# Optimization experiments

Measured on AMD Instinct MI355X. Metric: run time of the kernel, lower is better.

## Reference

```python
import jax, jax.numpy as jnp
import numpy as np

# Fixed production-scale sizes (equal-sized graphs so unbatch == reshape)
B, NQ, ND = 64, 32, 512     # graph pairs, query nodes/graph, data nodes/graph
DIN, D, K = 64, 128, 16     # GCN_in_size, GCN_out_size, NTN_k
DEG = 8                     # average degree


def _gcn(x, src, dst, W, b):
    """GCNConv with self loops + symmetric normalization (PyG semantics)."""
    N = x.shape[0]
    loop = jnp.arange(N)
    s = jnp.concatenate([src, loop])
    t = jnp.concatenate([dst, loop])
    deg = jax.ops.segment_sum(jnp.ones_like(t, x.dtype), t, num_segments=N)
    dinv = jnp.where(deg > 0, deg ** -0.5, 0.0)
    norm = (dinv[s] * dinv[t])[:, None]
    h = x @ W
    return jax.ops.segment_sum(h[s] * norm, t, num_segments=N) + b


def _three_gcn(x, ei, W1, b1, W2, b2, W3, b3):
    src, dst = ei[0], ei[1]
    h1 = jax.nn.relu(_gcn(x, src, dst, W1, b1))
    h2 = jax.nn.relu(_gcn(h1, src, dst, W2, b2))
    h3 = jax.nn.relu(_gcn(h2, src, dst, W3, b3))
    return h1, h2, h3


def _level(q, d, Wn, Vn, bn, cw, cb):
    """att_layer + NTN + elementwise mult + 1x1 conv + softmax over data nodes.
    q: [B,NQ,D], d: [B,ND,D] -> (softmaxed map [B,NQ,ND], raw map, he [B,K,NQ,ND])."""
    att = jax.nn.softmax(jnp.einsum('bqd,bnd->bqn', q, d) / jnp.sqrt(jnp.float32(D)), axis=-1)
    qW = jnp.einsum('bqd,kde->bkqe', q, Wn)           # [B,K,NQ,D]
    bil = jnp.einsum('bkqe,bne->bkqn', qW, d)          # [B,K,NQ,ND]
    lq = jnp.einsum('kd,bqd->bkq', Vn[:, :D], q)[:, :, :, None]
    ld = jnp.einsum('kd,bnd->bkn', Vn[:, D:], d)[:, :, None, :]
    he = jax.nn.sigmoid(bil + lq + ld + bn[None, :, None, None]) * att[:, None]
    e_raw = jnp.einsum('k,bkqn->bqn', cw, he) + cb     # 1x1 Conv2d(K->1)
    return jax.nn.softmax(e_raw, axis=-1), e_raw, he


def reference(x_d, edge_index_d, x_q, edge_index_q, batch_index_d, batch_index_q,
              W1, b1, W2, b2, W3, b3,
              Wn1, Vn1, bn1, cw1, cb1,
              Wn2, Vn2, bn2, cw2, cb2,
              Wn3, Vn3, bn3, cw3, cb3,
              w_end, b_end):
    d1, d2, d3 = _three_gcn(x_d, edge_index_d, W1, b1, W2, b2, W3, b3)
    q1, q2, q3 = _three_gcn(x_q, edge_index_q, W1, b1, W2, b2, W3, b3)
    # unbatch: batch indices are sorted with equal graph sizes -> reshape
    d1, d2, d3 = (t.reshape(B, ND, D) for t in (d1, d2, d3))
    q1, q2, q3 = (t.reshape(B, NQ, D) for t in (q1, q2, q3))
    e1, _, he1 = _level(q1, d1, Wn1, Vn1, bn1, cw1, cb1)
    _, e2raw, he2 = _level(q2, d2, Wn2, Vn2, bn2, cw2, cb2)
    e3, _, he3 = _level(q3, d3, Wn3, Vn3, bn3, cw3, cb3)
    # Faithful to source quirks: the zip unpack `e1,e2,e3,h1,h2,h1` rebinds h1 to
    # he_3 (he_1 is never used, he_3 appears twice) and end2 enters the concat
    # PRE-softmax (the softmaxed version was assigned to unused `nd2`).
    stack = jnp.concatenate([e1[:, None], e2raw[:, None], e3[:, None], he3, he2, he3], axis=1)
    out = jnp.einsum('c,bcqn->bqn', w_end, stack) + b_end  # con_end 1x1 conv + squeeze
    return jax.nn.softmax(out, axis=-1)                    # softmax over data nodes


def setup_inputs() -> dict:
    key = jax.random.key(0)
    k = jax.random.split(key, 40)
    n = jax.random.normal
    Nd, Nq = B * ND, B * NQ
    Ed, Eq = Nd * DEG, Nq * DEG
    gid_d = jnp.repeat(jnp.arange(B), ND * DEG)
    gid_q = jnp.repeat(jnp.arange(B), NQ * DEG)
    inp = {
        'x_d': n(k[0], (Nd, DIN), jnp.float32),
        'x_q': n(k[1], (Nq, DIN), jnp.float32),
        'edge_index_d': jnp.stack([jax.random.randint(k[2], (Ed,), 0, ND) + gid_d * ND,
                                   jax.random.randint(k[3], (Ed,), 0, ND) + gid_d * ND]),
        'edge_index_q': jnp.stack([jax.random.randint(k[4], (Eq,), 0, NQ) + gid_q * NQ,
                                   jax.random.randint(k[5], (Eq,), 0, NQ) + gid_q * NQ]),
        'batch_index_d': jnp.repeat(jnp.arange(B), ND),
        'batch_index_q': jnp.repeat(jnp.arange(B), NQ),
        'W1': n(k[6], (DIN, D), jnp.float32) / np.sqrt(DIN), 'b1': jnp.zeros((D,), jnp.float32),
        'W2': n(k[7], (D, D), jnp.float32) / np.sqrt(D), 'b2': jnp.zeros((D,), jnp.float32),
        'W3': n(k[8], (D, D), jnp.float32) / np.sqrt(D), 'b3': jnp.zeros((D,), jnp.float32),
    }
    for i, l in enumerate(('1', '2', '3')):
        inp['Wn' + l] = n(k[10 + 4 * i], (K, D, D), jnp.float32) / np.sqrt(D)
        inp['Vn' + l] = n(k[11 + 4 * i], (K, 2 * D), jnp.float32) / np.sqrt(2 * D)
        inp['bn' + l] = jnp.zeros((K,), jnp.float32)
        inp['cw' + l] = n(k[12 + 4 * i], (K,), jnp.float32) / np.sqrt(K)
        inp['cb' + l] = jnp.zeros((1,), jnp.float32)
    inp['w_end'] = n(k[25], (3 * K + 3,), jnp.float32) / np.sqrt(3 * K + 3)
    inp['b_end'] = jnp.zeros((1,), jnp.float32)
    return inp
```

## Files before the change

kernel.cpp:

```cpp
#include <hip/hip_runtime.h>
#include <math.h>

namespace {
constexpr int cB  = 64;
constexpr int cNQ = 32;
constexpr int cND = 512;
constexpr int cNd = cB * cND;
constexpr int cNq = cB * cNQ;
constexpr int cEd = cNd * 8;
constexpr int cEq = cNq * 8;
constexpr int LD_STRIDE = 516;
constexpr int NB_CSRD = 64;
constexpr int NB_CSRQ = 8;
constexpr int CVT0 = NB_CSRD + NB_CSRQ;
constexpr int NB_CVT = 2188;
constexpr int TR0 = CVT0 + NB_CVT;
constexpr int NB_T2BF = 808;
constexpr int GA_N = 4352;
constexpr int QW_N = 1024;
}

#define F4C(p) (*(const float4*)(p))

typedef __attribute__((ext_vector_type(8))) __bf16 bf16x8;
typedef __attribute__((ext_vector_type(4))) float floatx4;

__device__ __forceinline__ ushort f2bf(float f) {
  union { float f; unsigned u; } v;
  v.f = f;
  unsigned u = v.u;
  return (ushort)((u + 0x7fffu + ((u >> 16) & 1u)) >> 16);
}
__device__ __forceinline__ float bf2f(ushort u) {
  union { unsigned u; float f; } v;
  v.u = ((unsigned)u) << 16;
  return v.f;
}
__device__ __forceinline__ float4 us4f4(ushort4 u) {
  return make_float4(bf2f(u.x), bf2f(u.y), bf2f(u.z), bf2f(u.w));
}
__device__ __forceinline__ ushort4 f4us4(float4 f) {
  ushort4 o;
  o.x = f2bf(f.x); o.y = f2bf(f.y); o.z = f2bf(f.z); o.w = f2bf(f.w);
  return o;
}
__device__ __forceinline__ float fexp2(float x) {
#if __has_builtin(__builtin_amdgcn_exp2f)
  return __builtin_amdgcn_exp2f(x);
#else
  return exp2f(x);
#endif
}
__device__ __forceinline__ float frcp(float x) {
#if __has_builtin(__builtin_amdgcn_rcpf)
  return __builtin_amdgcn_rcpf(x);
#else
  return 1.0f / x;
#endif
}
__device__ __forceinline__ float fsigmoid(float z) {
  return frcp(1.0f + fexp2(z * -1.4426950408889634f));
}
__device__ __forceinline__ float fexp(float x) { return fexp2(x * 1.4426950408889634f); }

__device__ __forceinline__ int swz_g(int j) { return (((j >> 3) & 7) << 3) | (j & 7); }

__global__ __launch_bounds__(256) void k_front_csr(
    const float* __restrict__ xd, const float* __restrict__ xq,
    const float* __restrict__ v0, const float* __restrict__ v1,
    const float* __restrict__ v2, ushort* __restrict__ oxd, ushort* __restrict__ oxq,
    ushort* __restrict__ ov0, ushort* __restrict__ ov1, ushort* __restrict__ ov2,
    const float* __restrict__ W1, const float* __restrict__ W2,
    const float* __restrict__ W3, const float* __restrict__ Wn0,
    const float* __restrict__ Wn1, const float* __restrict__ Wn2,
    ushort* __restrict__ o1, ushort* __restrict__ o2, ushort* __restrict__ o3,
    ushort* __restrict__ on0, ushort* __restrict__ on1, ushort* __restrict__ on2,
    const int* __restrict__ src_d, const int* __restrict__ dst_d,
    const int* __restrict__ src_q, const int* __restrict__ dst_q,
    int* __restrict__ cnt_d, int* __restrict__ cnt_q,
    int* __restrict__ rp_d, int* __restrict__ rp_q,
    float* __restrict__ dinv_d, float* __restrict__ dinv_q,
    int* __restrict__ col_d, int* __restrict__ col_q) {
  __shared__ float tile[32][33];
  __shared__ int s_cnt[512];
  __shared__ int s_base[512];
  __shared__ int s_cur[512];
  int blk = blockIdx.x, tid = threadIdx.x;
  if (blk < NB_CSRD) {
    int g = blk;
    const int* dstg = dst_d + g * 4096;
    const int* srcg = src_d + g * 4096;
    int nbase = g * 512;
    s_cnt[tid] = 0; s_cnt[tid + 256] = 0;
    __syncthreads();
    for (int e = tid; e < 4096; e += 256) atomicAdd(&s_cnt[dstg[e] - nbase], 1);
    __syncthreads();
    int c0 = s_cnt[tid], c1 = s_cnt[tid + 256];
    s_base[tid] = c0; s_base[tid + 256] = c1;
    __syncthreads();
    for (int off = 1; off < 512; off <<= 1) {
      int a = (tid >= off) ? s_base[tid - off] : 0;
      int b = (tid + 256 >= off) ? s_base[tid + 256 - off] : 0;
      __syncthreads();
      s_base[tid] += a; s_base[tid + 256] += b;
      __syncthreads();
    }
    int e0 = s_base[tid] - c0, e1 = s_base[tid + 256] - c1;
    s_base[tid] = e0; s_base[tid + 256] = e1;
    s_cur[tid] = 0; s_cur[tid + 256] = 0;
    cnt_d[nbase + tid] = c0;
    cnt_d[nbase + tid + 256] = c1;
    rp_d[nbase + tid] = g * 4096 + e0;
    rp_d[nbase + tid + 256] = g * 4096 + e1;
    dinv_d[nbase + tid] = 1.0f / sqrtf((float)(c0 + 1));
    dinv_d[nbase + tid + 256] = 1.0f / sqrtf((float)(c1 + 1));
    __syncthreads();
    for (int e = tid; e < 4096; e += 256) {
      int d = dstg[e] - nbase;
      int p = atomicAdd(&s_cur[d], 1);
      col_d[g * 4096 + s_base[d] + p] = srcg[e];
    }
  } else if (blk < CVT0) {
    int qb = blk - NB_CSRD;
    int lg = tid >> 5, lane32 = tid & 31;
    int g = qb * 8 + lg;
    const int* dstg = dst_q + g * 256;
    const int* srcg = src_q + g * 256;
    int nbase = g * 32;
    s_cnt[tid] = 0;
    __syncthreads();
#pragma unroll
    for (int j = 0; j < 8; ++j)
      atomicAdd(&s_cnt[lg * 32 + (dstg[lane32 + j * 32] - nbase)], 1);
    __syncthreads();
    int v = s_cnt[tid];
    int incl = v;
#pragma unroll
    for (int off = 1; off < 32; off <<= 1) {
      int t = __shfl_up(incl, off, 32);
      if (lane32 >= off) incl += t;
    }
    int excl = incl - v;
    cnt_q[nbase + lane32] = v;
    rp_q[nbase + lane32] = g * 256 + excl;
    dinv_q[nbase + lane32] = 1.0f / sqrtf((float)(v + 1));
    s_base[tid] = excl;
    s_cur[tid] = 0;
    __syncthreads();
#pragma unroll
    for (int j = 0; j < 8; ++j) {
      int e = lane32 + j * 32;
      int d = dstg[e] - nbase;
      int p = atomicAdd(&s_cur[lg * 32 + d], 1);
      col_q[g * 256 + s_base[lg * 32 + d] + p] = srcg[e];
    }
  } else if (blk < TR0) {
    int b2 = blk - CVT0;
    const float* src;
    ushort* dst;
    int i;
    if (b2 < 2048) { src = xd; dst = oxd; i = b2 * 256 + tid; }
    else if (b2 < 2176) { src = xq; dst = oxq; i = (b2 - 2048) * 256 + tid; }
    else if (b2 < 2180) { src = v0; dst = ov0; i = (b2 - 2176) * 256 + tid; }
    else if (b2 < 2184) { src = v1; dst = ov1; i = (b2 - 2180) * 256 + tid; }
    else { src = v2; dst = ov2; i = (b2 - 2184) * 256 + tid; }
    *(ushort4*)(dst + (size_t)i * 4) = f4us4(F4C(src + (size_t)i * 4));
  } else {
    int b5 = blk - TR0;
    const float* in;
    ushort* out;
    int R, C, bt, t;
    if (b5 < 8)        { in = W1;  out = o1;  R = 64;  C = 128; bt = 0; t = b5; }
    else if (b5 < 24)  { in = W2;  out = o2;  R = 128; C = 128; bt = 0; t = b5 - 8; }
    else if (b5 < 40)  { in = W3;  out = o3;  R = 128; C = 128; bt = 0; t = b5 - 24; }
    else if (b5 < 296) { in = Wn0; out = on0; R = 128; C = 128; bt = (b5 - 40) >> 4;  t = (b5 - 40) & 15; }
    else if (b5 < 552) { in = Wn1; out = on1; R = 128; C = 128; bt = (b5 - 296) >> 4; t = (b5 - 296) & 15; }
    else               { in = Wn2; out = on2; R = 128; C = 128; bt = (b5 - 552) >> 4; t = (b5 - 552) & 15; }
    int tilesC = C >> 5;
    int tr = t / tilesC, tc = t - tr * tilesC;
    int tx = tid & 31, ty = tid >> 5;
    const float* ib = in + (size_t)bt * R * C;
    ushort* ob = out + (size_t)bt * R * C;
#pragma unroll
    for (int i = 0; i < 4; ++i)
      tile[ty + i * 8][tx] = ib[(tr * 32 + ty + i * 8) * C + tc * 32 + tx];
    __syncthreads();
#pragma unroll
    for (int i = 0; i < 4; ++i)
      ob[(size_t)(tc * 32 + ty + i * 8) * R + tr * 32 + tx] = f2bf(tile[tx][ty + i * 8]);
  }
}

__global__ __launch_bounds__(256) void k_gemm1(
    const ushort* __restrict__ xdbf, const ushort* __restrict__ xqbf,
    const ushort* __restrict__ w1T, const float* __restrict__ dinv_d,
    const float* __restrict__ dinv_q, ushort* __restrict__ htmp) {
  int blk2 = blockIdx.x, tid = threadIdx.x;
  int wave = tid >> 6, lane = tid & 63;
  int col = lane & 15, quad = lane >> 4;
  bool isQ = blk2 >= 512;
  int node0;
  if (isQ) node0 = (blk2 - 512) * 64;
  else node0 = swz_g(blk2) * 512 + (blk2 >> 6) * 64;
  int mloc = node0 + wave * 16;
  const ushort* X = isQ ? xqbf : xdbf;
  const float* dv = isQ ? dinv_q : dinv_d;
  size_t hbase = isQ ? (size_t)cNd : 0;
  floatx4 acc[8];
#pragma unroll
  for (int ct = 0; ct < 8; ++ct)
#pragma unroll
    for (int r = 0; r < 4; ++r) acc[ct][r] = 0.0f;
#pragma unroll
  for (int kc = 0; kc < 2; ++kc) {
    bf16x8 a = *(const bf16x8*)(X + (size_t)(mloc + col) * 64 + kc * 32 + quad * 8);
#pragma unroll
    for (int ct = 0; ct < 8; ++ct) {
      bf16x8 b = *(const bf16x8*)(w1T + (size_t)(ct * 16 + col) * 64 + kc * 32 + quad * 8);
      acc[ct] = __builtin_amdgcn_mfma_f32_16x16x32_bf16(a, b, acc[ct], 0, 0, 0);
    }
  }
  float sc[4];
#pragma unroll
  for (int r = 0; r < 4; ++r) sc[r] = dv[mloc + quad * 4 + r];
#pragma unroll
  for (int ct = 0; ct < 8; ++ct)
#pragma unroll
    for (int r = 0; r < 4; ++r)
      htmp[(hbase + mloc + quad * 4 + r) * 128 + ct * 16 + col] = f2bf(acc[ct][r] * sc[r]);
}

__global__ __launch_bounds__(256) void k_gather_qw(
    const ushort* __restrict__ htmp, const int* __restrict__ rp_d,
    const int* __restrict__ cnt_d, const int* __restrict__ col_d,
    const float* __restrict__ dinv_d, const int* __restrict__ rp_q,
    const int* __restrict__ cnt_q, const int* __restrict__ col_q,
    const float* __restrict__ dinv_q, const float* __restrict__ bias,
    ushort* __restrict__ dbf, ushort* __restrict__ qbf,
    const ushort* __restrict__ wnT, ushort* __restrict__ qw) {
  __shared__ ushort q_s[32 * 128];
  int blk = blockIdx.x, tid = threadIdx.x;
  if (blk < GA_N) {
    bool isQ = blk >= 4096;
    int node;
    if (isQ) {
      int j = blk - 4096;
      node = swz_g(j) * 32 + (j >> 6) * 8 + (tid >> 5);
    } else {
      node = swz_g(blk) * 512 + (blk >> 6) * 8 + (tid >> 5);
    }
    int l = tid & 31;
    const ushort* hs = htmp + (isQ ? (size_t)cNd * 128 : 0);
    const int* rp = isQ ? rp_q : rp_d;
    const int* cnt = isQ ? cnt_q : cnt_d;
    const int* col = isQ ? col_q : col_d;
    const float* dinv = isQ ? dinv_q : dinv_d;
    ushort* outp = isQ ? qbf : dbf;
    int c = cnt[node], s0 = rp[node];
    float dt = dinv[node];
    float4 acc = us4f4(*(const ushort4*)(hs + (size_t)node * 128 + l * 4));
    int cm = c < 32 ? c : 32;
    for (int j0 = 0; j0 < cm; j0 += 8) {
      int ss[8];
      ushort4 v[8];
#pragma unroll
      for (int t = 0; t < 8; ++t) {
        int jj = j0 + t;
        ss[t] = (jj < cm) ? col[s0 + jj] : -1;
      }
#pragma unroll
      for (int t = 0; t < 8; ++t)
        if (ss[t] >= 0) v[t] = *(const ushort4*)(hs + (size_t)ss[t] * 128 + l * 4);
#pragma unroll
      for (int t = 0; t < 8; ++t) {
        if (ss[t] >= 0) {
          float4 f = us4f4(v[t]);
          acc.x += f.x; acc.y += f.y; acc.z += f.z; acc.w += f.w;
        }
      }
    }
    for (int j = 32; j < c; ++j) {
      int s = col[s0 + j];
      float4 f = us4f4(*(const ushort4*)(hs + (size_t)s * 128 + l * 4));
      acc.x += f.x; acc.y += f.y; acc.z += f.z; acc.w += f.w;
    }
    float4 bv = F4C(bias + l * 4);
    float4 r;
    r.x = fmaxf(acc.x * dt + bv.x, 0.0f);
    r.y = fmaxf(acc.y * dt + bv.y, 0.0f);
    r.z = fmaxf(acc.z * dt + bv.z, 0.0f);
    r.w = fmaxf(acc.w * dt + bv.w, 0.0f);
    *(ushort4*)(outp + (size_t)node * 128 + l * 4) = f4us4(r);
    return;
  }
  int j = blk - GA_N;
  int b = swz_g(j & 63), k = j >> 6;
  {
    int n = tid >> 3, seg = tid & 7, d0 = seg * 16;
    int node = b * 32 + n;
    int c = cnt_q[node], s0 = rp_q[node];
    float dt = dinv_q[node];
    const ushort* hq = htmp + (size_t)cNd * 128;
    const ushort* own = hq + (size_t)node * 128 + d0;
    float4 a0 = us4f4(*(const ushort4*)(own));
    float4 a1 = us4f4(*(const ushort4*)(own + 4));
    float4 a2 = us4f4(*(const ushort4*)(own + 8));
    float4 a3 = us4f4(*(const ushort4*)(own + 12));
    for (int j2 = 0; j2 < c; ++j2) {
      int s = col_q[s0 + j2];
      const ushort* rr = hq + (size_t)s * 128 + d0;
      float4 f0 = us4f4(*(const ushort4*)(rr));
      float4 f1 = us4f4(*(const ushort4*)(rr + 4));
      float4 f2 = us4f4(*(const ushort4*)(rr + 8));
      float4 f3 = us4f4(*(const ushort4*)(rr + 12));
      a0.x += f0.x; a0.y += f0.y; a0.z += f0.z; a0.w += f0.w;
      a1.x += f1.x; a1.y += f1.y; a1.z += f1.z; a1.w += f1.w;
      a2.x += f2.x; a2.y += f2.y; a2.z += f2.z; a2.w += f2.w;
      a3.x += f3.x; a3.y += f3.y; a3.z += f3.z; a3.w += f3.w;
    }
    float4 bv0 = F4C(bias + d0), bv1 = F4C(bias + d0 + 4);
    float4 bv2 = F4C(bias + d0 + 8), bv3 = F4C(bias + d0 + 12);
    float4 r0, r1, r2, r3;
    r0.x = fmaxf(a0.x * dt + bv0.x, 0.0f); r0.y = fmaxf(a0.y * dt + bv0.y, 0.0f);
    r0.z = fmaxf(a0.z * dt + bv0.z, 0.0f); r0.w = fmaxf(a0.w * dt + bv0.w, 0.0f);
    r1.x = fmaxf(a1.x * dt + bv1.x, 0.0f); r1.y = fmaxf(a1.y * dt + bv1.y, 0.0f);
    r1.z = fmaxf(a1.z * dt + bv1.z, 0.0f); r1.w = fmaxf(a1.w * dt + bv1.w, 0.0f);
    r2.x = fmaxf(a2.x * dt + bv2.x, 0.0f); r2.y = fmaxf(a2.y * dt + bv2.y, 0.0f);
    r2.z = fmaxf(a2.z * dt + bv2.z, 0.0f); r2.w = fmaxf(a2.w * dt + bv2.w, 0.0f);
    r3.x = fmaxf(a3.x * dt + bv3.x, 0.0f); r3.y = fmaxf(a3.y * dt + bv3.y, 0.0f);
    r3.z = fmaxf(a3.z * dt + bv3.z, 0.0f); r3.w = fmaxf(a3.w * dt + bv3.w, 0.0f);
    ushort4 u0 = f4us4(r0), u1 = f4us4(r1), u2 = f4us4(r2), u3 = f4us4(r3);
    char* qsb = (char*)q_s;
    int x0 = (n * 256 + d0 * 2) ^ ((n & 7) << 4);
    int x1 = (n * 256 + d0 * 2 + 16) ^ ((n & 7) << 4);
    *(ushort4*)(qsb + x0) = u0;
    *(ushort4*)(qsb + x0 + 8) = u1;
    *(ushort4*)(qsb + x1) = u2;
    *(ushort4*)(qsb + x1 + 8) = u3;
  }
  __syncthreads();
  int wave = tid >> 6, lane = tid & 63;
  int col = lane & 15, quad = lane >> 4;
  int et0 = wave * 2;
  const char* qsb = (const char*)q_s;
  floatx4 acc[2][2];
#pragma unroll
  for (int qt = 0; qt < 2; ++qt)
#pragma unroll
    for (int ei = 0; ei < 2; ++ei)
#pragma unroll
      for (int r = 0; r < 4; ++r) acc[qt][ei][r] = 0.0f;
#pragma unroll
  for (int kc = 0; kc < 4; ++kc) {
    int r0 = col, r1 = 16 + col;
    bf16x8 a0 = *(const bf16x8*)(qsb + ((r0 * 256 + kc * 64 + quad * 16) ^ ((r0 & 7) << 4)));
    bf16x8 a1 = *(const bf16x8*)(qsb + ((r1 * 256 + kc * 64 + quad * 16) ^ ((r1 & 7) << 4)));
#pragma unroll
    for (int ei = 0; ei < 2; ++ei) {
      bf16x8 bf = *(const bf16x8*)(wnT + (size_t)(k * 128 + (et0 + ei) * 16 + col) * 128 +
                                   kc * 32 + quad * 8);
      acc[0][ei] = __builtin_amdgcn_mfma_f32_16x16x32_bf16(a0, bf, acc[0][ei], 0, 0, 0);
      acc[1][ei] = __builtin_amdgcn_mfma_f32_16x16x32_bf16(a1, bf, acc[1][ei], 0, 0, 0);
    }
  }
#pragma unroll
  for (int qt = 0; qt < 2; ++qt)
#pragma unroll
    for (int ei = 0; ei < 2; ++ei)
#pragma unroll
      for (int r = 0; r < 4; ++r)
        qw[((size_t)(b * 16 + k) << 12) + (qt * 16 + quad * 4 + r) * 128 +
           (et0 + ei) * 16 + col] = f2bf(acc[qt][ei][r]);
}

__global__ __launch_bounds__(512, 2) void k_level_gemm(
    const ushort* __restrict__ qbf, const ushort* __restrict__ dbf,
    const ushort* __restrict__ qw, const ushort* __restrict__ vnbf,
    const float* __restrict__ bn, const float* __restrict__ cw,
    const float* __restrict__ w_end, const float* __restrict__ b_end,
    int o1, int o2, int hasF, int do_sm, int mode, int widx,
    float* __restrict__ accb, float* __restrict__ out,
    const ushort* __restrict__ gWT, const float* __restrict__ dinv_d,
    const float* __restrict__ dinv_q, ushort* __restrict__ htmp) {
  __shared__ float s_ld[16 * LD_STRIDE];
  __shared__ float s_lq[16 * 16];
  __shared__ float s_red[16 * 8];
  int tid = threadIdx.x;
  int wave = tid >> 6, lane = tid & 63;
  int col = lane & 15, quad = lane >> 4;

  if (blockIdx.x >= 128) {
    int gblk = blockIdx.x - 128;
    bool isQ = gblk >= 256;
    int node0;
    if (isQ) node0 = (gblk - 256) * 128;
    else node0 = swz_g(gblk) * 512 + (gblk >> 6) * 128;
    int mloc = node0 + wave * 16;
    const ushort* X = isQ ? qbf : dbf;
    const float* dv = isQ ? dinv_q : dinv_d;
    size_t hbase = isQ ? (size_t)cNd : 0;
    floatx4 acc[8];
#pragma unroll
    for (int ct = 0; ct < 8; ++ct)
#pragma unroll
      for (int r = 0; r < 4; ++r) acc[ct][r] = 0.0f;
#pragma unroll
    for (int kc = 0; kc < 4; ++kc) {
      bf16x8 a = *(const bf16x8*)(X + (size_t)(mloc + col) * 128 + kc * 32 + quad * 8);
#pragma unroll
      for (int ct = 0; ct < 8; ++ct) {
        bf16x8 b = *(const bf16x8*)(gWT + (size_t)(ct * 16 + col) * 128 + kc * 32 + quad * 8);
        acc[ct] = __builtin_amdgcn_mfma_f32_16x16x32_bf16(a, b, acc[ct], 0, 0, 0);
      }
    }
    float sc[4];
#pragma unroll
    for (int r = 0; r < 4; ++r) sc[r] = dv[mloc + quad * 4 + r];
#pragma unroll
    for (int ct = 0; ct < 8; ++ct)
#pragma unroll
      for (int r = 0; r < 4; ++r)
        htmp[(hbase + mloc + quad * 4 + r) * 128 + ct * 16 + col] = f2bf(acc[ct][r] * sc[r]);
    return;
  }

  int b = swz_g(blockIdx.x & 63);
  int qh = blockIdx.x >> 6;
  int n0 = wave * 64;

  bf16x8 bfr[4][4];
#pragma unroll
  for (int s = 0; s < 4; ++s)
#pragma unroll
    for (int kc = 0; kc < 4; ++kc)
      bfr[s][kc] = *(const bf16x8*)(dbf + ((size_t)(b * 512 + n0 + s * 16 + col) << 7) +
                                    kc * 32 + quad * 8);
  bf16x8 aq[4];
#pragma unroll
  for (int kc = 0; kc < 4; ++kc)
    aq[kc] = *(const bf16x8*)(qbf + (size_t)(b * 32 + qh * 16 + col) * 128 +
                              kc * 32 + quad * 8);

  floatx4 att[4];
#pragma unroll
  for (int s = 0; s < 4; ++s)
#pragma unroll
    for (int r = 0; r < 4; ++r) att[s][r] = 0.0f;
#pragma unroll
  for (int kc = 0; kc < 4; ++kc)
#pragma unroll
    for (int s = 0; s < 4; ++s)
      att[s] = __builtin_amdgcn_mfma_f32_16x16x32_bf16(aq[kc], bfr[s][kc], att[s], 0, 0, 0);
  const float sc = 0.088388347648318440550f;
#pragma unroll
  for (int s = 0; s < 4; ++s)
#pragma unroll
    for (int r = 0; r < 4; ++r) att[s][r] *= sc;

  {
    bf16x8 vn2[4];
#pragma unroll
    for (int kc = 0; kc < 4; ++kc)
      vn2[kc] = *(const bf16x8*)(vnbf + col * 256 + 128 + kc * 32 + quad * 8);
#pragma unroll
    for (int s = 0; s < 4; ++s) {
      floatx4 lda;
#pragma unroll
      for (int r = 0; r < 4; ++r) lda[r] = 0.0f;
#pragma unroll
      for (int kc = 0; kc < 4; ++kc)
        lda = __builtin_amdgcn_mfma_f32_16x16x32_bf16(bfr[s][kc], vn2[kc], lda, 0, 0, 0);
#pragma unroll
      for (int r = 0; r < 4; ++r)
        s_ld[col * LD_STRIDE + n0 + s * 16 + quad * 4 + r] = lda[r];
    }
  }
  if (wave == 0) {
    bf16x8 vn1[4];
#pragma unroll
    for (int kc = 0; kc < 4; ++kc)
      vn1[kc] = *(const bf16x8*)(vnbf + col * 256 + kc * 32 + quad * 8);
    floatx4 lqa;
#pragma unroll
    for (int r = 0; r < 4; ++r) lqa[r] = 0.0f;
#pragma unroll
    for (int kc = 0; kc < 4; ++kc)
      lqa = __builtin_amdgcn_mfma_f32_16x16x32_bf16(aq[kc], vn1[kc], lqa, 0, 0, 0);
#pragma unroll
    for (int r = 0; r < 4; ++r) s_lq[col * 16 + quad * 4 + r] = lqa[r];
  }
  __syncthreads();

  float red[4], M[4];
#pragma unroll
  for (int r = 0; r < 4; ++r) {
    float m = fmaxf(fmaxf(att[0][r], att[1][r]), fmaxf(att[2][r], att[3][r]));
#pragma unroll
    for (int o = 1; o < 16; o <<= 1) m = fmaxf(m, __shfl_xor(m, o, 64));
    red[r] = m;
  }
  if (col == 0)
#pragma unroll
    for (int r = 0; r < 4; ++r) s_red[(quad * 4 + r) * 8 + wave] = red[r];
  __syncthreads();
#pragma unroll
  for (int r = 0; r < 4; ++r) {
    float m = s_red[(quad * 4 + r) * 8];
#pragma unroll
    for (int w = 1; w < 8; ++w) m = fmaxf(m, s_red[(quad * 4 + r) * 8 + w]);
    M[r] = m;
  }
  __syncthreads();
#pragma unroll
  for (int s = 0; s < 4; ++s)
#pragma unroll
    for (int r = 0; r < 4; ++r) att[s][r] = fexp(att[s][r] - M[r]);
#pragma unroll
  for (int r = 0; r < 4; ++r) {
    float m = att[0][r] + att[1][r] + att[2][r] + att[3][r];
#pragma unroll
    for (int o = 1; o < 16; o <<= 1) m += __shfl_xor(m, o, 64);
    red[r] = m;
  }
  if (col == 0)
#pragma unroll
    for (int r = 0; r < 4; ++r) s_red[(quad * 4 + r) * 8 + wave] = red[r];
  __syncthreads();
#pragma unroll
  for (int r = 0; r < 4; ++r) {
    float m = s_red[(quad * 4 + r) * 8];
#pragma unroll
    for (int w = 1; w < 8; ++w) m += s_red[(quad * 4 + r) * 8 + w];
    M[r] = frcp(m);
  }
  __syncthreads();
#pragma unroll
  for (int s = 0; s < 4; ++s)
#pragma unroll
    for (int r = 0; r < 4; ++r) att[s][r] *= M[r];

  floatx4 eacc[4], facc[4];
#pragma unroll
  for (int s = 0; s < 4; ++s)
#pragma unroll
    for (int r = 0; r < 4; ++r) { eacc[s][r] = 0.0f; facc[s][r] = 0.0f; }

#pragma unroll 4
  for (int k = 0; k < 16; ++k) {
    const ushort* qk = qw + ((size_t)(b * 16 + k) << 12) + (qh * 16 + col) * 128 + quad * 8;
    bf16x8 a0 = *(const bf16x8*)(qk);
    bf16x8 a1 = *(const bf16x8*)(qk + 32);
    bf16x8 a2 = *(const bf16x8*)(qk + 64);
    bf16x8 a3 = *(const bf16x8*)(qk + 96);
    floatx4 bil[4];
#pragma unroll
    for (int s = 0; s < 4; ++s) {
#pragma unroll
      for (int r = 0; r < 4; ++r) bil[s][r] = 0.0f;
      bil[s] = __builtin_amdgcn_mfma_f32_16x16x32_bf16(a0, bfr[s][0], bil[s], 0, 0, 0);
      bil[s] = __builtin_amdgcn_mfma_f32_16x16x32_bf16(a1, bfr[s][1], bil[s], 0, 0, 0);
      bil[s] = __builtin_amdgcn_mfma_f32_16x16x32_bf16(a2, bfr[s][2], bil[s], 0, 0, 0);
      bil[s] = __builtin_amdgcn_mfma_f32_16x16x32_bf16(a3, bfr[s][3], bil[s], 0, 0, 0);
    }
    float bnk = bn[k], cwk = cw[k];
    float wkk = 0.0f;
    if (hasF) {
      wkk = w_end[o1 + k];
      if (o2 >= 0) wkk += w_end[o2 + k];
    }
    float lqv[4];
#pragma unroll
    for (int r = 0; r < 4; ++r) lqv[r] = s_lq[k * 16 + quad * 4 + r] + bnk;
#pragma unroll
    for (int s = 0; s < 4; ++s) {
      float ldv = s_ld[k * LD_STRIDE + n0 + s * 16 + col];
#pragma unroll
      for (int r = 0; r < 4; ++r) {
        float sg = fsigmoid(bil[s][r] + lqv[r] + ldv);
        eacc[s][r] += cwk * sg;
        facc[s][r] += wkk * sg;
      }
    }
  }

#pragma unroll
  for (int s = 0; s < 4; ++s)
#pragma unroll
    for (int r = 0; r < 4; ++r) {
      eacc[s][r] *= att[s][r];
      facc[s][r] *= att[s][r];
    }
  if (do_sm) {
#pragma unroll
    for (int r = 0; r < 4; ++r) {
      float m = fmaxf(fmaxf(eacc[0][r], eacc[1][r]), fmaxf(eacc[2][r], eacc[3][r]));
#pragma unroll
      for (int o = 1; o < 16; o <<= 1) m = fmaxf(m, __shfl_xor(m, o, 64));
      red[r] = m;
    }
    if (col == 0)
#pragma unroll
      for (int r = 0; r < 4; ++r) s_red[(quad * 4 + r) * 8 + wave] = red[r];
    __syncthreads();
#pragma unroll
    for (int r = 0; r < 4; ++r) {
      float m = s_red[(quad * 4 + r) * 8];
#pragma unroll
      for (int w = 1; w < 8; ++w) m = fmaxf(m, s_red[(quad * 4 + r) * 8 + w]);
      M[r] = m;
    }
    __syncthreads();
#pragma unroll
    for (int s = 0; s < 4; ++s)
#pragma unroll
      for (int r = 0; r < 4; ++r) eacc[s][r] = fexp(eacc[s][r] - M[r]);
#pragma unroll
    for (int r = 0; r < 4; ++r) {
      float m = eacc[0][r] + eacc[1][r] + eacc[2][r] + eacc[3][r];
#pragma unroll
      for (int o = 1; o < 16; o <<= 1) m += __shfl_xor(m, o, 64);
      red[r] = m;
    }
    if (col == 0)
#pragma unroll
      for (int r = 0; r < 4; ++r) s_red[(quad * 4 + r) * 8 + wave] = red[r];
    __syncthreads();
#pragma unroll
    for (int r = 0; r < 4; ++r) {
      float m = s_red[(quad * 4 + r) * 8];
#pragma unroll
      for (int w = 1; w < 8; ++w) m += s_red[(quad * 4 + r) * 8 + w];
      M[r] = frcp(m);
    }
    __syncthreads();
#pragma unroll
    for (int s = 0; s < 4; ++s)
#pragma unroll
      for (int r = 0; r < 4; ++r) eacc[s][r] *= M[r];
  }
  float w = w_end[widx];
#pragma unroll
  for (int s = 0; s < 4; ++s)
#pragma unroll
    for (int r = 0; r < 4; ++r) eacc[s][r] = w * eacc[s][r] + (hasF ? facc[s][r] : 0.0f);

  if (mode == 0) {
#pragma unroll
    for (int s = 0; s < 4; ++s)
#pragma unroll
      for (int r = 0; r < 4; ++r)
        accb[((size_t)(b * 32 + qh * 16 + quad * 4 + r) << 9) + n0 + s * 16 + col] =
            eacc[s][r];
  } else if (mode == 1) {
#pragma unroll
    for (int s = 0; s < 4; ++s)
#pragma unroll
      for (int r = 0; r < 4; ++r)
        accb[((size_t)(b * 32 + qh * 16 + quad * 4 + r) << 9) + n0 + s * 16 + col] +=
            eacc[s][r];
  } else {
    float be = b_end[0];
#pragma unroll
    for (int s = 0; s < 4; ++s)
#pragma unroll
      for (int r = 0; r < 4; ++r)
        eacc[s][r] += accb[((size_t)(b * 32 + qh * 16 + quad * 4 + r) << 9) +
                           n0 + s * 16 + col] + be;
#pragma unroll
    for (int r = 0; r < 4; ++r) {
      float m = fmaxf(fmaxf(eacc[0][r], eacc[1][r]), fmaxf(eacc[2][r], eacc[3][r]));
#pragma unroll
      for (int o = 1; o < 16; o <<= 1) m = fmaxf(m, __shfl_xor(m, o, 64));
      red[r] = m;
    }
    if (col == 0)
#pragma unroll
      for (int r = 0; r < 4; ++r) s_red[(quad * 4 + r) * 8 + wave] = red[r];
    __syncthreads();
#pragma unroll
    for (int r = 0; r < 4; ++r) {
      float m = s_red[(quad * 4 + r) * 8];
#pragma unroll
      for (int w2 = 1; w2 < 8; ++w2) m = fmaxf(m, s_red[(quad * 4 + r) * 8 + w2]);
      M[r] = m;
    }
    __syncthreads();
#pragma unroll
    for (int s = 0; s < 4; ++s)
#pragma unroll
      for (int r = 0; r < 4; ++r) eacc[s][r] = fexp(eacc[s][r] - M[r]);
#pragma unroll
    for (int r = 0; r < 4; ++r) {
      float m = eacc[0][r] + eacc[1][r] + eacc[2][r] + eacc[3][r];
#pragma unroll
      for (int o = 1; o < 16; o <<= 1) m += __shfl_xor(m, o, 64);
      red[r] = m;
    }
    if (col == 0)
#pragma unroll
      for (int r = 0; r < 4; ++r) s_red[(quad * 4 + r) * 8 + wave] = red[r];
    __syncthreads();
#pragma unroll
    for (int r = 0; r < 4; ++r) {
      float m = s_red[(quad * 4 + r) * 8];
#pragma unroll
      for (int w2 = 1; w2 < 8; ++w2) m += s_red[(quad * 4 + r) * 8 + w2];
      M[r] = frcp(m);
    }
#pragma unroll
    for (int s = 0; s < 4; ++s)
#pragma unroll
      for (int r = 0; r < 4; ++r)
        out[((size_t)(b * 32 + qh * 16 + quad * 4 + r) << 9) + n0 + s * 16 + col] =
            eacc[s][r] * M[r];
  }
}

extern "C" void kernel_launch(void* const* d_in, const int* in_sizes, int n_in,
                              void* d_out, int out_size, void* d_ws, size_t ws_size,
                              hipStream_t stream) {
  (void)in_sizes; (void)n_in; (void)out_size; (void)ws_size;
  const float* x_d = (const float*)d_in[0];
  const float* x_q = (const float*)d_in[1];
  const int* ei_d = (const int*)d_in[2];
  const int* ei_q = (const int*)d_in[3];
  const float* W1 = (const float*)d_in[6];
  const float* b1 = (const float*)d_in[7];
  const float* W2 = (const float*)d_in[8];
  const float* b2 = (const float*)d_in[9];
  const float* W3 = (const float*)d_in[10];
  const float* b3 = (const float*)d_in[11];
  const float* Wn[3] = {(const float*)d_in[12], (const float*)d_in[17], (const float*)d_in[22]};
  const float* Vn[3] = {(const float*)d_in[13], (const float*)d_in[18], (const float*)d_in[23]};
  const float* bn[3] = {(const float*)d_in[14], (const float*)d_in[19], (const float*)d_in[24]};
  const float* cw[3] = {(const float*)d_in[15], (const float*)d_in[20], (const float*)d_in[25]};
  const float* w_end = (const float*)d_in[27];
  const float* b_end = (const float*)d_in[28];
  float* out = (float*)d_out;

  char* wsp = (char*)d_ws;
  auto alloc = [&](size_t nbytes) {
    void* p = (void*)wsp;
    wsp += (nbytes + 255) & ~(size_t)255;
    return p;
  };
  int* cnt_d = (int*)alloc(cNd * 4);
  int* cnt_q = (int*)alloc(cNq * 4);
  float* dinv_d = (float*)alloc(cNd * 4);
  float* dinv_q = (float*)alloc(cNq * 4);
  int* rp_d = (int*)alloc(cNd * 4);
  int* rp_q = (int*)alloc(cNq * 4);
  int* col_d = (int*)alloc((size_t)cEd * 4);
  int* col_q = (int*)alloc((size_t)cEq * 4);
  ushort* xdbf = (ushort*)alloc((size_t)cNd * 64 * 2);
  ushort* xqbf = (ushort*)alloc((size_t)cNq * 64 * 2);
  ushort* w1T = (ushort*)alloc(128 * 64 * 2);
  ushort* w2T = (ushort*)alloc(128 * 128 * 2);
  ushort* w3T = (ushort*)alloc(128 * 128 * 2);
  ushort* wnT[3];
  for (int l = 0; l < 3; ++l) wnT[l] = (ushort*)alloc((size_t)16 * 128 * 128 * 2);
  ushort* vnbf[3];
  for (int l = 0; l < 3; ++l) vnbf[l] = (ushort*)alloc(16 * 256 * 2);
  ushort* htmp = (ushort*)alloc((size_t)(cNd + cNq) * 128 * 2);
  ushort* dbf = (ushort*)alloc((size_t)cNd * 128 * 2);
  ushort* qbf[3];
  for (int l = 0; l < 3; ++l) qbf[l] = (ushort*)alloc((size_t)cNq * 128 * 2);
  float* accb = (float*)alloc((size_t)cB * cNQ * cND * 4);
  ushort* qwbuf = (ushort*)alloc((size_t)cB * 16 * 32 * 128 * 2);

  const int* src_d = ei_d;
  const int* dst_d = ei_d + cEd;
  const int* src_q = ei_q;
  const int* dst_q = ei_q + cEq;

  k_front_csr<<<TR0 + NB_T2BF, 256, 0, stream>>>(
      x_d, x_q, Vn[0], Vn[1], Vn[2], xdbf, xqbf, vnbf[0], vnbf[1], vnbf[2], W1, W2,
      W3, Wn[0], Wn[1], Wn[2], w1T, w2T, w3T, wnT[0], wnT[1], wnT[2],
      src_d, dst_d, src_q, dst_q, cnt_d, cnt_q, rp_d, rp_q, dinv_d, dinv_q,
      col_d, col_q);

  k_gemm1<<<544, 256, 0, stream>>>(xdbf, xqbf, w1T, dinv_d, dinv_q, htmp);

  const float* bias[3] = {b1, b2, b3};
  const ushort* nextWT[3] = {w2T, w3T, nullptr};
  const int o1s[3] = {0, 19, 3};
  const int o2s[3] = {-1, -1, 35};
  const int hasF[3] = {0, 1, 1};
  const int dosms[3] = {1, 0, 1};
  const int modes[3] = {0, 1, 2};

  for (int l = 0; l < 3; ++l) {
    k_gather_qw<<<GA_N + QW_N, 256, 0, stream>>>(
        htmp, rp_d, cnt_d, col_d, dinv_d, rp_q, cnt_q, col_q, dinv_q, bias[l], dbf,
        qbf[l], wnT[l], qwbuf);
    int grid = (l < 2) ? (128 + 272) : 128;
    k_level_gemm<<<grid, 512, 0, stream>>>(
        qbf[l], dbf, qwbuf, vnbf[l], bn[l], cw[l], w_end, b_end, o1s[l], o2s[l],
        hasF[l], dosms[l], modes[l], l, accb, out, nextWT[l], dinv_d, dinv_q, htmp);
  }
}
```

Baseline: 305.3 us.

## Compute query aggregation once per graph and loop NTN slices inside QW blocks

```diff
diff --git a/kernel.cpp b/kernel.cpp
--- a/kernel.cpp
+++ b/kernel.cpp
@@ -16,8 +16,8 @@
 constexpr int NB_CVT = 2188;
 constexpr int TR0 = CVT0 + NB_CVT;
 constexpr int NB_T2BF = 808;
-constexpr int GA_N = 4352;
-constexpr int QW_N = 1024;
+constexpr int NB_QW = 64;
+constexpr int NB_GAD = 4096;
 }
 
 #define F4C(p) (*(const float4*)(p))
@@ -240,25 +240,13 @@
     const ushort* __restrict__ wnT, ushort* __restrict__ qw) {
   __shared__ ushort q_s[32 * 128];
   int blk = blockIdx.x, tid = threadIdx.x;
-  if (blk < GA_N) {
-    bool isQ = blk >= 4096;
-    int node;
-    if (isQ) {
-      int j = blk - 4096;
-      node = swz_g(j) * 32 + (j >> 6) * 8 + (tid >> 5);
-    } else {
-      node = swz_g(blk) * 512 + (blk >> 6) * 8 + (tid >> 5);
-    }
+  if (blk >= NB_QW) {
+    int j = blk - NB_QW;
+    int node = swz_g(j) * 512 + (j >> 6) * 8 + (tid >> 5);
     int l = tid & 31;
-    const ushort* hs = htmp + (isQ ? (size_t)cNd * 128 : 0);
-    const int* rp = isQ ? rp_q : rp_d;
-    const int* cnt = isQ ? cnt_q : cnt_d;
-    const int* col = isQ ? col_q : col_d;
-    const float* dinv = isQ ? dinv_q : dinv_d;
-    ushort* outp = isQ ? qbf : dbf;
-    int c = cnt[node], s0 = rp[node];
-    float dt = dinv[node];
-    float4 acc = us4f4(*(const ushort4*)(hs + (size_t)node * 128 + l * 4));
+    int c = cnt_d[node], s0 = rp_d[node];
+    float dt = dinv_d[node];
+    float4 acc = us4f4(*(const ushort4*)(htmp + (size_t)node * 128 + l * 4));
     int cm = c < 32 ? c : 32;
     for (int j0 = 0; j0 < cm; j0 += 8) {
       int ss[8];
@@ -266,11 +254,11 @@
 #pragma unroll
       for (int t = 0; t < 8; ++t) {
         int jj = j0 + t;
-        ss[t] = (jj < cm) ? col[s0 + jj] : -1;
+        ss[t] = (jj < cm) ? col_d[s0 + jj] : -1;
       }
 #pragma unroll
       for (int t = 0; t < 8; ++t)
-        if (ss[t] >= 0) v[t] = *(const ushort4*)(hs + (size_t)ss[t] * 128 + l * 4);
+        if (ss[t] >= 0) v[t] = *(const ushort4*)(htmp + (size_t)ss[t] * 128 + l * 4);
 #pragma unroll
       for (int t = 0; t < 8; ++t) {
         if (ss[t] >= 0) {
@@ -279,9 +267,9 @@
         }
       }
     }
-    for (int j = 32; j < c; ++j) {
-      int s = col[s0 + j];
-      float4 f = us4f4(*(const ushort4*)(hs + (size_t)s * 128 + l * 4));
+    for (int j2 = 32; j2 < c; ++j2) {
+      int s = col_d[s0 + j2];
+      float4 f = us4f4(*(const ushort4*)(htmp + (size_t)s * 128 + l * 4));
       acc.x += f.x; acc.y += f.y; acc.z += f.z; acc.w += f.w;
     }
     float4 bv = F4C(bias + l * 4);
@@ -290,11 +278,10 @@
     r.y = fmaxf(acc.y * dt + bv.y, 0.0f);
     r.z = fmaxf(acc.z * dt + bv.z, 0.0f);
     r.w = fmaxf(acc.w * dt + bv.w, 0.0f);
-    *(ushort4*)(outp + (size_t)node * 128 + l * 4) = f4us4(r);
+    *(ushort4*)(dbf + (size_t)node * 128 + l * 4) = f4us4(r);
     return;
   }
-  int j = blk - GA_N;
-  int b = swz_g(j & 63), k = j >> 6;
+  int b = swz_g(blk);
   {
     int n = tid >> 3, seg = tid & 7, d0 = seg * 16;
     int node = b * 32 + n;
@@ -330,6 +317,10 @@
     r3.x = fmaxf(a3.x * dt + bv3.x, 0.0f); r3.y = fmaxf(a3.y * dt + bv3.y, 0.0f);
     r3.z = fmaxf(a3.z * dt + bv3.z, 0.0f); r3.w = fmaxf(a3.w * dt + bv3.w, 0.0f);
     ushort4 u0 = f4us4(r0), u1 = f4us4(r1), u2 = f4us4(r2), u3 = f4us4(r3);
+    *(ushort4*)(qbf + (size_t)node * 128 + d0) = u0;
+    *(ushort4*)(qbf + (size_t)node * 128 + d0 + 4) = u1;
+    *(ushort4*)(qbf + (size_t)node * 128 + d0 + 8) = u2;
+    *(ushort4*)(qbf + (size_t)node * 128 + d0 + 12) = u3;
     char* qsb = (char*)q_s;
     int x0 = (n * 256 + d0 * 2) ^ ((n & 7) << 4);
     int x1 = (n * 256 + d0 * 2 + 16) ^ ((n & 7) << 4);
@@ -343,34 +334,40 @@
   int col = lane & 15, quad = lane >> 4;
   int et0 = wave * 2;
   const char* qsb = (const char*)q_s;
-  floatx4 acc[2][2];
-#pragma unroll
-  for (int qt = 0; qt < 2; ++qt)
-#pragma unroll
-    for (int ei = 0; ei < 2; ++ei)
-#pragma unroll
-      for (int r = 0; r < 4; ++r) acc[qt][ei][r] = 0.0f;
+  bf16x8 qa0[4], qa1[4];
 #pragma unroll
   for (int kc = 0; kc < 4; ++kc) {
     int r0 = col, r1 = 16 + col;
-    bf16x8 a0 = *(const bf16x8*)(qsb + ((r0 * 256 + kc * 64 + quad * 16) ^ ((r0 & 7) << 4)));
-    bf16x8 a1 = *(const bf16x8*)(qsb + ((r1 * 256 + kc * 64 + quad * 16) ^ ((r1 & 7) << 4)));
-#pragma unroll
-    for (int ei = 0; ei < 2; ++ei) {
-      bf16x8 bf = *(const bf16x8*)(wnT + (size_t)(k * 128 + (et0 + ei) * 16 + col) * 128 +
-                                   kc * 32 + quad * 8);
-      acc[0][ei] = __builtin_amdgcn_mfma_f32_16x16x32_bf16(a0, bf, acc[0][ei], 0, 0, 0);
-      acc[1][ei] = __builtin_amdgcn_mfma_f32_16x16x32_bf16(a1, bf, acc[1][ei], 0, 0, 0);
-    }
-  }
-#pragma unroll
-  for (int qt = 0; qt < 2; ++qt)
-#pragma unroll
-    for (int ei = 0; ei < 2; ++ei)
-#pragma unroll
-      for (int r = 0; r < 4; ++r)
-        qw[((size_t)(b * 16 + k) << 12) + (qt * 16 + quad * 4 + r) * 128 +
-           (et0 + ei) * 16 + col] = f2bf(acc[qt][ei][r]);
+    qa0[kc] = *(const bf16x8*)(qsb + ((r0 * 256 + kc * 64 + quad * 16) ^ ((r0 & 7) << 4)));
+    qa1[kc] = *(const bf16x8*)(qsb + ((r1 * 256 + kc * 64 + quad * 16) ^ ((r1 & 7) << 4)));
+  }
+  for (int k = 0; k < 16; ++k) {
+    floatx4 acc[2][2];
+#pragma unroll
+    for (int qt = 0; qt < 2; ++qt)
+#pragma unroll
+      for (int ei = 0; ei < 2; ++ei)
+#pragma unroll
+        for (int r = 0; r < 4; ++r) acc[qt][ei][r] = 0.0f;
+#pragma unroll
+    for (int kc = 0; kc < 4; ++kc) {
+#pragma unroll
+      for (int ei = 0; ei < 2; ++ei) {
+        bf16x8 bf = *(const bf16x8*)(wnT + (size_t)(k * 128 + (et0 + ei) * 16 + col) * 128 +
+                                     kc * 32 + quad * 8);
+        acc[0][ei] = __builtin_amdgcn_mfma_f32_16x16x32_bf16(qa0[kc], bf, acc[0][ei], 0, 0, 0);
+        acc[1][ei] = __builtin_amdgcn_mfma_f32_16x16x32_bf16(qa1[kc], bf, acc[1][ei], 0, 0, 0);
+      }
+    }
+#pragma unroll
+    for (int qt = 0; qt < 2; ++qt)
+#pragma unroll
+      for (int ei = 0; ei < 2; ++ei)
+#pragma unroll
+        for (int r = 0; r < 4; ++r)
+          qw[((size_t)(b * 16 + k) << 12) + (qt * 16 + quad * 4 + r) * 128 +
+             (et0 + ei) * 16 + col] = f2bf(acc[qt][ei][r]);
+  }
 }
 
 __global__ __launch_bounds__(512, 2) void k_level_gemm(
@@ -790,7 +787,7 @@
   const int modes[3] = {0, 1, 2};
 
   for (int l = 0; l < 3; ++l) {
-    k_gather_qw<<<GA_N + QW_N, 256, 0, stream>>>(
+    k_gather_qw<<<NB_QW + NB_GAD, 256, 0, stream>>>(
         htmp, rp_d, cnt_d, col_d, dinv_d, rp_q, cnt_q, col_q, dinv_q, bias[l], dbf,
         qbf[l], wnT[l], qwbuf);
     int grid = (l < 2) ? (128 + 272) : 128;
```

After: 324.1 us. 1.06x slower.
